# Performance work log

Measured on AMD Instinct MI355X. Metric: run time of the kernel, lower is better.

## Reference

```python
import jax, jax.numpy as jnp
import numpy as np

N_ITEMS = 100000
H = 256
L = 3
B = 512


def setup_inputs() -> dict:
    key = jax.random.key(0)
    ks = jax.random.split(key, 9)
    s = 1.0 / np.sqrt(H)  # PyTorch GRU/Linear default uniform bound
    return {
        "input": jax.random.randint(ks[0], (B,), 0, N_ITEMS),
        "hidden": jnp.zeros((L, B, H), jnp.float32),
        "W_ih0": jax.random.uniform(ks[1], (3 * H, N_ITEMS), jnp.float32, -s, s),
        "W_ih_hi": jax.random.uniform(ks[2], (L - 1, 3 * H, H), jnp.float32, -s, s),
        "W_hh": jax.random.uniform(ks[3], (L, 3 * H, H), jnp.float32, -s, s),
        "b_ih": jax.random.uniform(ks[4], (L, 3 * H), jnp.float32, -s, s),
        "b_hh": jax.random.uniform(ks[5], (L, 3 * H), jnp.float32, -s, s),
        "W_out": jax.random.uniform(ks[6], (N_ITEMS, H), jnp.float32, -s, s),
        "b_out": jax.random.uniform(ks[7], (N_ITEMS,), jnp.float32, -s, s),
    }


def _gru_cell(x_proj, h, W_hh_l, b_hh_l):
    # PyTorch GRU cell; x_proj already holds x @ W_ih.T + b_ih
    h_proj = h @ W_hh_l.T + b_hh_l
    xr, xz, xn = jnp.split(x_proj, 3, axis=-1)
    hr, hz, hn = jnp.split(h_proj, 3, axis=-1)
    r = jax.nn.sigmoid(xr + hr)
    z = jax.nn.sigmoid(xz + hz)
    n = jnp.tanh(xn + r * hn)
    return (1.0 - z) * n + z * h


def reference(input, hidden, W_ih0, W_ih_hi, W_hh, b_ih, b_hh, W_out, b_out):
    # one_hot(input) @ W_ih0.T == row-gather of W_ih0.T  (same math, no dense one-hot)
    x_proj = W_ih0.T[input] + b_ih[0]  # (B, 3H)
    x = _gru_cell(x_proj, hidden[0], W_hh[0], b_hh[0])
    new_h = [x]
    for l in range(1, L):  # fixed small layer loop
        x_proj = x @ W_ih_hi[l - 1].T + b_ih[l]
        x = _gru_cell(x_proj, hidden[l], W_hh[l], b_hh[l])
        new_h.append(x)
    h_new = jnp.stack(new_h)  # (L, B, H)
    activation = jnp.tanh(x @ W_out.T + b_out)  # (B, N_ITEMS)
    return activation, h_new
```

## Files before the change

### kernel.cpp

```cpp
#include <hip/hip_runtime.h>
#include <math.h>
#include <stdint.h>

#define NI 100000
#define NB 512
#define NH 256
#define H3 768

typedef _Float16 f16x8 __attribute__((ext_vector_type(8)));
typedef float    f32x4 __attribute__((ext_vector_type(4)));

__device__ __forceinline__ float tanh_fast(float x) {
    x = fminf(fmaxf(x, -9.0f), 9.0f);
    const float e = __expf(2.0f * x);
    return (e - 1.0f) * __builtin_amdgcn_rcpf(e + 1.0f);
}

__global__ void k_gates0(const int* __restrict__ idx,
                         const float* __restrict__ Wih0,
                         const float* __restrict__ bih0,
                         const float* __restrict__ hp,
                         const float* __restrict__ hprev,
                         float* __restrict__ hnew)
{
    const int b = blockIdx.x;
    const int j = threadIdx.x;
    const int ib = idx[b];
    const float xr = Wih0[(size_t)(j          ) * NI + ib] + bih0[j];
    const float xz = Wih0[(size_t)(j + NH     ) * NI + ib] + bih0[j + NH];
    const float xn = Wih0[(size_t)(j + 2 * NH ) * NI + ib] + bih0[j + 2 * NH];
    const float hr = hp[b * H3 + j];
    const float hz = hp[b * H3 + NH + j];
    const float hn = hp[b * H3 + 2 * NH + j];
    const float h  = hprev[b * NH + j];
    const float r = 1.0f / (1.0f + expf(-(xr + hr)));
    const float z = 1.0f / (1.0f + expf(-(xz + hz)));
    const float n = tanhf(xn + r * hn);
    hnew[b * NH + j] = (1.0f - z) * n + z * h;
}

__global__ void k_gates(const float* __restrict__ xp,
                        const float* __restrict__ hp,
                        const float* __restrict__ hprev,
                        float* __restrict__ hnew)
{
    const int b = blockIdx.x;
    const int j = threadIdx.x;
    const float xr = xp[b * H3 + j];
    const float xz = xp[b * H3 + NH + j];
    const float xn = xp[b * H3 + 2 * NH + j];
    const float hr = hp[b * H3 + j];
    const float hz = hp[b * H3 + NH + j];
    const float hn = hp[b * H3 + 2 * NH + j];
    const float h  = hprev[b * NH + j];
    const float r = 1.0f / (1.0f + expf(-(xr + hr)));
    const float z = 1.0f / (1.0f + expf(-(xz + hz)));
    const float n = tanhf(xn + r * hn);
    hnew[b * NH + j] = (1.0f - z) * n + z * h;
}

__global__ void k_gates_last(const float* __restrict__ xp,
                             const float* __restrict__ hp,
                             const float* __restrict__ hprev,
                             float* __restrict__ hnew,
                             _Float16* __restrict__ Xh)
{
    const int b = blockIdx.x;
    const int j = threadIdx.x;
    const float xr = xp[b * H3 + j];
    const float xz = xp[b * H3 + NH + j];
    const float xn = xp[b * H3 + 2 * NH + j];
    const float hr = hp[b * H3 + j];
    const float hz = hp[b * H3 + NH + j];
    const float hn = hp[b * H3 + 2 * NH + j];
    const float h  = hprev[b * NH + j];
    const float r = 1.0f / (1.0f + expf(-(xr + hr)));
    const float z = 1.0f / (1.0f + expf(-(xz + hz)));
    const float n = tanhf(xn + r * hn);
    const float v = (1.0f - z) * n + z * h;
    hnew[b * NH + j] = v;
    Xh[b * NH + j] = (_Float16)v;
}

__global__ __launch_bounds__(256)
void k_gemm_small(const float* __restrict__ A0,
                  const float* __restrict__ B0,
                  const float* __restrict__ bias0,
                  float* __restrict__ C0,
                  int M, int N, int K,
                  int sA, int sB, int sBias, int sC)
{
    constexpr int BM = 64, BN = 64, BK = 64;
    __shared__ float As[BK][BM];
    __shared__ float Bs[BK][BN];

    const float* A    = A0 + (size_t)blockIdx.z * sA;
    const float* Bm   = B0 + (size_t)blockIdx.z * sB;
    const float* bias = bias0 + (size_t)blockIdx.z * sBias;
    float*       C    = C0 + (size_t)blockIdx.z * sC;

    const int tid = threadIdx.x;
    const int tx  = tid & 15;
    const int ty  = tid >> 4;
    const int m0  = blockIdx.x * BM;
    const int n0  = blockIdx.y * BN;

    float acc[4][4];
#pragma unroll
    for (int i = 0; i < 4; i++)
#pragma unroll
        for (int j = 0; j < 4; j++) acc[i][j] = 0.0f;

    for (int k0 = 0; k0 < K; k0 += BK) {
#pragma unroll
        for (int f = 0; f < 4; f++) {
            const int fid = tid + f * 256;
            const int row = fid >> 4;
            const int t4  = fid & 15;
            const int mp  = row ^ ((t4 & 3) << 3);
            {
                const float4 v = *(const float4*)(A + (size_t)(m0 + row) * K + k0 + t4 * 4);
                As[t4 * 4 + 0][mp] = v.x; As[t4 * 4 + 1][mp] = v.y;
                As[t4 * 4 + 2][mp] = v.z; As[t4 * 4 + 3][mp] = v.w;
            }
            {
                const float4 v = *(const float4*)(Bm + (size_t)(n0 + row) * K + k0 + t4 * 4);
                Bs[t4 * 4 + 0][mp] = v.x; Bs[t4 * 4 + 1][mp] = v.y;
                Bs[t4 * 4 + 2][mp] = v.z; Bs[t4 * 4 + 3][mp] = v.w;
            }
        }
        __syncthreads();
#pragma unroll
        for (int kk = 0; kk < BK; kk++) {
            const int s = ((kk >> 2) & 3) << 3;
            const float4 a0 = *(const float4*)&As[kk][(ty * 4) ^ s];
            const float4 b0 = *(const float4*)&Bs[kk][(tx * 4) ^ s];
            const float av[4] = {a0.x, a0.y, a0.z, a0.w};
            const float bv[4] = {b0.x, b0.y, b0.z, b0.w};
#pragma unroll
            for (int i = 0; i < 4; i++)
#pragma unroll
                for (int j = 0; j < 4; j++)
                    acc[i][j] = fmaf(av[i], bv[j], acc[i][j]);
        }
        __syncthreads();
    }

#pragma unroll
    for (int i = 0; i < 4; i++) {
        const size_t rowoff = (size_t)(m0 + ty * 4 + i) * N;
        const int gn = n0 + tx * 4;
        const float4 bb = *(const float4*)(bias + gn);
        float4 v;
        v.x = acc[i][0] + bb.x; v.y = acc[i][1] + bb.y;
        v.z = acc[i][2] + bb.z; v.w = acc[i][3] + bb.w;
        *(float4*)(C + rowoff + gn) = v;
    }
}

__global__ __launch_bounds__(512, 4)
void k_out_mfma(const _Float16* __restrict__ Xh,
                const float* __restrict__ W,
                const float* __restrict__ bout,
                float* __restrict__ C)
{
    __shared__ __align__(16) float S[16384];

    const int n0   = blockIdx.x * 64;
    const int tid  = threadIdx.x;
    const int w    = tid >> 6;
    const int lane = tid & 63;
    const int lr   = lane & 15;
    const int lg   = lane >> 4;

#pragma unroll
    for (int it = 0; it < 8; ++it) {
        const int fid = it * 512 + tid;
        const int row = fid >> 6;
        const int p   = fid & 63;
        int gr = n0 + row; if (gr >= NI) gr = NI - 1;
        const float* src = W + (size_t)gr * NH + (size_t)(p ^ (row & 7)) * 4;
        __builtin_amdgcn_global_load_lds(
            (const __attribute__((address_space(1))) void*)src,
            (__attribute__((address_space(3))) void*)(S + fid * 4),
            16, 0, 0);
    }

    f32x4 acc[4][4];
#pragma unroll
    for (int nf = 0; nf < 4; ++nf)
#pragma unroll
        for (int mf = 0; mf < 4; ++mf) acc[nf][mf] = (f32x4){0.f, 0.f, 0.f, 0.f};

    __syncthreads();

    const _Float16* xbase = Xh + (size_t)(w * 64 + lr) * NH + lg * 8;

#pragma unroll
    for (int t = 0; t < 8; ++t) {
        f16x8 xf[4];
#pragma unroll
        for (int mf = 0; mf < 4; ++mf)
            xf[mf] = *(const f16x8*)(xbase + mf * 16 * NH + t * 32);
#pragma unroll
        for (int nf = 0; nf < 4; ++nf) {
            const int rl = nf * 16 + lr;
            const int c0 = t * 8 + ((lg * 2)     ^ (rl & 7));
            const int c1 = t * 8 + ((lg * 2 + 1) ^ (rl & 7));
            const f32x4 u0 = *(const f32x4*)(S + rl * 256 + c0 * 4);
            const f32x4 u1 = *(const f32x4*)(S + rl * 256 + c1 * 4);
            f16x8 h;
            h[0] = (_Float16)u0[0]; h[1] = (_Float16)u0[1];
            h[2] = (_Float16)u0[2]; h[3] = (_Float16)u0[3];
            h[4] = (_Float16)u1[0]; h[5] = (_Float16)u1[1];
            h[6] = (_Float16)u1[2]; h[7] = (_Float16)u1[3];
#pragma unroll
            for (int mf = 0; mf < 4; ++mf)
                acc[nf][mf] = __builtin_amdgcn_mfma_f32_16x16x32_f16(
                    h, xf[mf], acc[nf][mf], 0, 0, 0);
        }
    }

#pragma unroll
    for (int pass = 0; pass < 2; ++pass) {
        __syncthreads();
        if ((w >> 2) == pass) {
            const int mloc = (w & 3) * 64;
#pragma unroll
            for (int nf = 0; nf < 4; ++nf) {
                const int gn = n0 + nf * 16 + lg * 4;
                const float4 bb = (gn < NI) ? *(const float4*)(bout + gn)
                                            : make_float4(0.f, 0.f, 0.f, 0.f);
#pragma unroll
                for (int mf = 0; mf < 4; ++mf) {
                    const int mr = mloc + mf * 16 + lr;
                    const int p  = (nf * 4 + lg) ^ (lr & 7);
                    float4 v;
                    v.x = tanh_fast(acc[nf][mf][0] + bb.x);
                    v.y = tanh_fast(acc[nf][mf][1] + bb.y);
                    v.z = tanh_fast(acc[nf][mf][2] + bb.z);
                    v.w = tanh_fast(acc[nf][mf][3] + bb.w);
                    *(float4*)(S + mr * 64 + p * 4) = v;
                }
            }
        }
        __syncthreads();
#pragma unroll
        for (int it = 0; it < 8; ++it) {
            const int fid = it * 512 + tid;
            const int row = fid >> 4;
            const int c   = fid & 15;
            const int gn  = n0 + c * 4;
            if (gn < NI) {
                const f32x4 v = *(const f32x4*)(S + row * 64 + ((c ^ (row & 7)) * 4));
                __builtin_nontemporal_store(
                    v, (f32x4*)(C + (size_t)(pass * 256 + row) * NI + gn));
            }
        }
    }
}

extern "C" void kernel_launch(void* const* d_in, const int* in_sizes, int n_in,
                              void* d_out, int out_size, void* d_ws, size_t ws_size,
                              hipStream_t stream)
{
    const int*   idx    = (const int*)  d_in[0];
    const float* hidden = (const float*)d_in[1];
    const float* Wih0   = (const float*)d_in[2];
    const float* WihHi  = (const float*)d_in[3];
    const float* Whh    = (const float*)d_in[4];
    const float* bih    = (const float*)d_in[5];
    const float* bhh    = (const float*)d_in[6];
    const float* Wout   = (const float*)d_in[7];
    const float* bout   = (const float*)d_in[8];

    float* act  = (float*)d_out;
    float* hnew = act + (size_t)NB * NI;
    float* hp = act;
    float* xp = act + 3 * NB * H3;
    _Float16* Xh = (_Float16*)d_ws;

    const dim3 bs(256);
    const dim3 gs_hp(NB / 64, H3 / 64, 3);
    const dim3 gs_xp(NB / 64, H3 / 64, 1);

    k_gemm_small<<<gs_hp, bs, 0, stream>>>(hidden, Whh, bhh, hp,
                                           NB, H3, NH, NB * NH, H3 * NH, H3, NB * H3);
    k_gates0<<<NB, bs, 0, stream>>>(idx, Wih0, bih, hp, hidden, hnew);
    k_gemm_small<<<gs_xp, bs, 0, stream>>>(hnew, WihHi, bih + H3, xp,
                                           NB, H3, NH, 0, 0, 0, 0);
    k_gates<<<NB, bs, 0, stream>>>(xp, hp + NB * H3, hidden + NB * NH, hnew + NB * NH);
    k_gemm_small<<<gs_xp, bs, 0, stream>>>(hnew + NB * NH, WihHi + H3 * NH, bih + 2 * H3, xp,
                                           NB, H3, NH, 0, 0, 0, 0);
    k_gates_last<<<NB, bs, 0, stream>>>(xp, hp + 2 * NB * H3, hidden + 2 * NB * NH,
                                        hnew + 2 * NB * NH, Xh);

    k_out_mfma<<<dim3((NI + 63) / 64), dim3(512), 0, stream>>>(Xh, Wout, bout, act);
}
```

Before: 148.3 us.

## Fuse GRU gate math into layer GEMMs and retile output MFMA warps

Folds the layer-0 and layer-1 gate computations into the A-tile load of the following input-projection GEMM, removing two kernel launches and the round-trip of hnew through global memory. Each of the 12 column blocks recomputes the gates redundantly, and for layer 0 that includes strided gathers from the large embedding matrix. It also switches gate math to fast exp/tanh approximations. The output MFMA kernel is retiled so each warp covers 128 rows by 32 columns instead of 64 by 64, which cuts per-warp LDS weight reads and fp16 conversions but means more Xh loads from global.

```diff
diff --git a/kernel.cpp b/kernel.cpp
--- a/kernel.cpp
+++ b/kernel.cpp
@@ -15,34 +15,15 @@
     const float e = __expf(2.0f * x);
     return (e - 1.0f) * __builtin_amdgcn_rcpf(e + 1.0f);
 }
-
-__global__ void k_gates0(const int* __restrict__ idx,
-                         const float* __restrict__ Wih0,
-                         const float* __restrict__ bih0,
-                         const float* __restrict__ hp,
-                         const float* __restrict__ hprev,
-                         float* __restrict__ hnew)
-{
-    const int b = blockIdx.x;
-    const int j = threadIdx.x;
-    const int ib = idx[b];
-    const float xr = Wih0[(size_t)(j          ) * NI + ib] + bih0[j];
-    const float xz = Wih0[(size_t)(j + NH     ) * NI + ib] + bih0[j + NH];
-    const float xn = Wih0[(size_t)(j + 2 * NH ) * NI + ib] + bih0[j + 2 * NH];
-    const float hr = hp[b * H3 + j];
-    const float hz = hp[b * H3 + NH + j];
-    const float hn = hp[b * H3 + 2 * NH + j];
-    const float h  = hprev[b * NH + j];
-    const float r = 1.0f / (1.0f + expf(-(xr + hr)));
-    const float z = 1.0f / (1.0f + expf(-(xz + hz)));
-    const float n = tanhf(xn + r * hn);
-    hnew[b * NH + j] = (1.0f - z) * n + z * h;
-}
-
-__global__ void k_gates(const float* __restrict__ xp,
-                        const float* __restrict__ hp,
-                        const float* __restrict__ hprev,
-                        float* __restrict__ hnew)
+__device__ __forceinline__ float sigmoid_fast(float x) {
+    return 1.0f / (1.0f + __expf(-x));
+}
+
+__global__ void k_gates_last(const float* __restrict__ xp,
+                             const float* __restrict__ hp,
+                             const float* __restrict__ hprev,
+                             float* __restrict__ hnew,
+                             _Float16* __restrict__ Xh)
 {
     const int b = blockIdx.x;
     const int j = threadIdx.x;
@@ -53,30 +34,9 @@
     const float hz = hp[b * H3 + NH + j];
     const float hn = hp[b * H3 + 2 * NH + j];
     const float h  = hprev[b * NH + j];
-    const float r = 1.0f / (1.0f + expf(-(xr + hr)));
-    const float z = 1.0f / (1.0f + expf(-(xz + hz)));
-    const float n = tanhf(xn + r * hn);
-    hnew[b * NH + j] = (1.0f - z) * n + z * h;
-}
-
-__global__ void k_gates_last(const float* __restrict__ xp,
-                             const float* __restrict__ hp,
-                             const float* __restrict__ hprev,
-                             float* __restrict__ hnew,
-                             _Float16* __restrict__ Xh)
-{
-    const int b = blockIdx.x;
-    const int j = threadIdx.x;
-    const float xr = xp[b * H3 + j];
-    const float xz = xp[b * H3 + NH + j];
-    const float xn = xp[b * H3 + 2 * NH + j];
-    const float hr = hp[b * H3 + j];
-    const float hz = hp[b * H3 + NH + j];
-    const float hn = hp[b * H3 + 2 * NH + j];
-    const float h  = hprev[b * NH + j];
-    const float r = 1.0f / (1.0f + expf(-(xr + hr)));
-    const float z = 1.0f / (1.0f + expf(-(xz + hz)));
-    const float n = tanhf(xn + r * hn);
+    const float r = sigmoid_fast(xr + hr);
+    const float z = sigmoid_fast(xz + hz);
+    const float n = tanh_fast(xn + r * hn);
     const float v = (1.0f - z) * n + z * h;
     hnew[b * NH + j] = v;
     Xh[b * NH + j] = (_Float16)v;
@@ -158,6 +118,119 @@
     }
 }
 
+template<int MODE>
+__global__ __launch_bounds__(256)
+void k_gemm_fused(const int* __restrict__ idx,
+                  const float* __restrict__ Wih0,
+                  const float* __restrict__ bih0,
+                  const float* __restrict__ xprev,
+                  const float* __restrict__ hpl,
+                  const float* __restrict__ hprev,
+                  const float* __restrict__ Bm,
+                  const float* __restrict__ bias,
+                  float* __restrict__ hnew_out,
+                  float* __restrict__ xp_out)
+{
+    constexpr int BM = 64, BN = 64, BK = 64;
+    __shared__ float As[BK][BM];
+    __shared__ float Bs[BK][BN];
+
+    const int tid = threadIdx.x;
+    const int tx  = tid & 15;
+    const int ty  = tid >> 4;
+    const int m0  = blockIdx.x * BM;
+    const int n0  = blockIdx.y * BN;
+
+    float acc[4][4];
+#pragma unroll
+    for (int i = 0; i < 4; i++)
+#pragma unroll
+        for (int j = 0; j < 4; j++) acc[i][j] = 0.0f;
+
+    for (int k0 = 0; k0 < NH; k0 += BK) {
+#pragma unroll
+        for (int f = 0; f < 4; f++) {
+            const int fid = tid + f * 256;
+            const int row = fid >> 4;
+            const int t4  = fid & 15;
+            const int mp  = row ^ ((t4 & 3) << 3);
+            const int b   = m0 + row;
+            const int j0  = k0 + t4 * 4;
+
+            float xr[4], xz[4], xn[4];
+            if (MODE == 0) {
+                const int ib = idx[b];
+#pragma unroll
+                for (int e = 0; e < 4; e++) {
+                    xr[e] = Wih0[(size_t)(j0 + e) * NI + ib]          + bih0[j0 + e];
+                    xz[e] = Wih0[(size_t)(j0 + e + NH) * NI + ib]     + bih0[j0 + e + NH];
+                    xn[e] = Wih0[(size_t)(j0 + e + 2 * NH) * NI + ib] + bih0[j0 + e + 2 * NH];
+                }
+            } else {
+                const float4 a = *(const float4*)(xprev + (size_t)b * H3 + j0);
+                const float4 c = *(const float4*)(xprev + (size_t)b * H3 + NH + j0);
+                const float4 d = *(const float4*)(xprev + (size_t)b * H3 + 2 * NH + j0);
+                xr[0]=a.x; xr[1]=a.y; xr[2]=a.z; xr[3]=a.w;
+                xz[0]=c.x; xz[1]=c.y; xz[2]=c.z; xz[3]=c.w;
+                xn[0]=d.x; xn[1]=d.y; xn[2]=d.z; xn[3]=d.w;
+            }
+            const float4 hr4 = *(const float4*)(hpl + (size_t)b * H3 + j0);
+            const float4 hz4 = *(const float4*)(hpl + (size_t)b * H3 + NH + j0);
+            const float4 hn4 = *(const float4*)(hpl + (size_t)b * H3 + 2 * NH + j0);
+            const float4 h4  = *(const float4*)(hprev + (size_t)b * NH + j0);
+            const float hr[4] = {hr4.x, hr4.y, hr4.z, hr4.w};
+            const float hz[4] = {hz4.x, hz4.y, hz4.z, hz4.w};
+            const float hn[4] = {hn4.x, hn4.y, hn4.z, hn4.w};
+            const float hh[4] = {h4.x, h4.y, h4.z, h4.w};
+            float av[4];
+#pragma unroll
+            for (int e = 0; e < 4; e++) {
+                const float r = sigmoid_fast(xr[e] + hr[e]);
+                const float z = sigmoid_fast(xz[e] + hz[e]);
+                const float n = tanh_fast(xn[e] + r * hn[e]);
+                av[e] = (1.0f - z) * n + z * hh[e];
+            }
+            As[t4 * 4 + 0][mp] = av[0]; As[t4 * 4 + 1][mp] = av[1];
+            As[t4 * 4 + 2][mp] = av[2]; As[t4 * 4 + 3][mp] = av[3];
+            if (n0 == 0) {
+                float4 o; o.x = av[0]; o.y = av[1]; o.z = av[2]; o.w = av[3];
+                *(float4*)(hnew_out + (size_t)b * NH + j0) = o;
+            }
+            {
+                const float4 v = *(const float4*)(Bm + (size_t)(n0 + row) * NH + k0 + t4 * 4);
+                Bs[t4 * 4 + 0][mp] = v.x; Bs[t4 * 4 + 1][mp] = v.y;
+                Bs[t4 * 4 + 2][mp] = v.z; Bs[t4 * 4 + 3][mp] = v.w;
+            }
+        }
+        __syncthreads();
+#pragma unroll
+        for (int kk = 0; kk < BK; kk++) {
+            const int s = ((kk >> 2) & 3) << 3;
+            const float4 a0 = *(const float4*)&As[kk][(ty * 4) ^ s];
+            const float4 b0 = *(const float4*)&Bs[kk][(tx * 4) ^ s];
+            const float av[4] = {a0.x, a0.y, a0.z, a0.w};
+            const float bv[4] = {b0.x, b0.y, b0.z, b0.w};
+#pragma unroll
+            for (int i = 0; i < 4; i++)
+#pragma unroll
+                for (int j = 0; j < 4; j++)
+                    acc[i][j] = fmaf(av[i], bv[j], acc[i][j]);
+        }
+        __syncthreads();
+    }
+
+#pragma unroll
+    for (int i = 0; i < 4; i++) {
+        const size_t rowoff = (size_t)(m0 + ty * 4 + i) * H3;
+        const int gn = n0 + tx * 4;
+        const float4 bb = *(const float4*)(bias + gn);
+        float4 v;
+        v.x = acc[i][0] + bb.x; v.y = acc[i][1] + bb.y;
+        v.z = acc[i][2] + bb.z; v.w = acc[i][3] + bb.w;
+        *(float4*)(xp_out + rowoff + gn) = v;
+    }
+}
+
 __global__ __launch_bounds__(512, 4)
 void k_out_mfma(const _Float16* __restrict__ Xh,
                 const float* __restrict__ W,
@@ -172,39 +245,39 @@
     const int lane = tid & 63;
     const int lr   = lane & 15;
     const int lg   = lane >> 4;
+    const int p    = w >> 2;
+    const int wmh  = (w >> 1) & 1;
+    const int wn2  = w & 1;
 
 #pragma unroll
     for (int it = 0; it < 8; ++it) {
         const int fid = it * 512 + tid;
         const int row = fid >> 6;
-        const int p   = fid & 63;
+        const int pc  = fid & 63;
         int gr = n0 + row; if (gr >= NI) gr = NI - 1;
-        const float* src = W + (size_t)gr * NH + (size_t)(p ^ (row & 7)) * 4;
+        const float* src = W + (size_t)gr * NH + (size_t)(pc ^ (row & 7)) * 4;
         __builtin_amdgcn_global_load_lds(
             (const __attribute__((address_space(1))) void*)src,
             (__attribute__((address_space(3))) void*)(S + fid * 4),
             16, 0, 0);
     }
 
-    f32x4 acc[4][4];
-#pragma unroll
-    for (int nf = 0; nf < 4; ++nf)
-#pragma unroll
-        for (int mf = 0; mf < 4; ++mf) acc[nf][mf] = (f32x4){0.f, 0.f, 0.f, 0.f};
+    f32x4 acc[2][8];
+#pragma unroll
+    for (int nf = 0; nf < 2; ++nf)
+#pragma unroll
+        for (int mf = 0; mf < 8; ++mf) acc[nf][mf] = (f32x4){0.f, 0.f, 0.f, 0.f};
 
     __syncthreads();
 
-    const _Float16* xbase = Xh + (size_t)(w * 64 + lr) * NH + lg * 8;
+    const _Float16* xbase = Xh + (size_t)(p * 256 + wmh * 128 + lr) * NH + lg * 8;
 
 #pragma unroll
     for (int t = 0; t < 8; ++t) {
-        f16x8 xf[4];
-#pragma unroll
-        for (int mf = 0; mf < 4; ++mf)
-            xf[mf] = *(const f16x8*)(xbase + mf * 16 * NH + t * 32);
-#pragma unroll
-        for (int nf = 0; nf < 4; ++nf) {
-            const int rl = nf * 16 + lr;
+        f16x8 wf[2];
+#pragma unroll
+        for (int nf = 0; nf < 2; ++nf) {
+            const int rl = wn2 * 32 + nf * 16 + lr;
             const int c0 = t * 8 + ((lg * 2)     ^ (rl & 7));
             const int c1 = t * 8 + ((lg * 2 + 1) ^ (rl & 7));
             const f32x4 u0 = *(const f32x4*)(S + rl * 256 + c0 * 4);
@@ -214,33 +287,36 @@
             h[2] = (_Float16)u0[2]; h[3] = (_Float16)u0[3];
             h[4] = (_Float16)u1[0]; h[5] = (_Float16)u1[1];
             h[6] = (_Float16)u1[2]; h[7] = (_Float16)u1[3];
-#pragma unroll
-            for (int mf = 0; mf < 4; ++mf)
-                acc[nf][mf] = __builtin_amdgcn_mfma_f32_16x16x32_f16(
-                    h, xf[mf], acc[nf][mf], 0, 0, 0);
+            wf[nf] = h;
+        }
+#pragma unroll
+        for (int mf = 0; mf < 8; ++mf) {
+            const f16x8 xf = *(const f16x8*)(xbase + mf * 16 * NH + t * 32);
+            acc[0][mf] = __builtin_amdgcn_mfma_f32_16x16x32_f16(wf[0], xf, acc[0][mf], 0, 0, 0);
+            acc[1][mf] = __builtin_amdgcn_mfma_f32_16x16x32_f16(wf[1], xf, acc[1][mf], 0, 0, 0);
         }
     }
 
 #pragma unroll
     for (int pass = 0; pass < 2; ++pass) {
         __syncthreads();
-        if ((w >> 2) == pass) {
-            const int mloc = (w & 3) * 64;
-#pragma unroll
-            for (int nf = 0; nf < 4; ++nf) {
-                const int gn = n0 + nf * 16 + lg * 4;
+        if (p == pass) {
+#pragma unroll
+            for (int nf = 0; nf < 2; ++nf) {
+                const int gn = n0 + wn2 * 32 + nf * 16 + lg * 4;
                 const float4 bb = (gn < NI) ? *(const float4*)(bout + gn)
                                             : make_float4(0.f, 0.f, 0.f, 0.f);
-#pragma unroll
-                for (int mf = 0; mf < 4; ++mf) {
-                    const int mr = mloc + mf * 16 + lr;
-                    const int p  = (nf * 4 + lg) ^ (lr & 7);
+                const int q = wn2 * 8 + nf * 4 + lg;
+#pragma unroll
+                for (int mf = 0; mf < 8; ++mf) {
+                    const int mr   = wmh * 128 + mf * 16 + lr;
+                    const int slot = q ^ (lr & 7);
                     float4 v;
                     v.x = tanh_fast(acc[nf][mf][0] + bb.x);
                     v.y = tanh_fast(acc[nf][mf][1] + bb.y);
                     v.z = tanh_fast(acc[nf][mf][2] + bb.z);
                     v.w = tanh_fast(acc[nf][mf][3] + bb.w);
-                    *(float4*)(S + mr * 64 + p * 4) = v;
+                    *(float4*)(S + mr * 64 + slot * 4) = v;
                 }
             }
         }
@@ -276,8 +352,9 @@
 
     float* act  = (float*)d_out;
     float* hnew = act + (size_t)NB * NI;
-    float* hp = act;
-    float* xp = act + 3 * NB * H3;
+    float* hp  = act;
+    float* xp1 = act + 3 * NB * H3;
+    float* xp2 = xp1 + NB * H3;
     _Float16* Xh = (_Float16*)d_ws;
 
     const dim3 bs(256);
@@ -286,14 +363,14 @@
 
     k_gemm_small<<<gs_hp, bs, 0, stream>>>(hidden, Whh, bhh, hp,
                                            NB, H3, NH, NB * NH, H3 * NH, H3, NB * H3);
-    k_gates0<<<NB, bs, 0, stream>>>(idx, Wih0, bih, hp, hidden, hnew);
-    k_gemm_small<<<gs_xp, bs, 0, stream>>>(hnew, WihHi, bih + H3, xp,
-                                           NB, H3, NH, 0, 0, 0, 0);
-    k_gates<<<NB, bs, 0, stream>>>(xp, hp + NB * H3, hidden + NB * NH, hnew + NB * NH);
-    k_gemm_small<<<gs_xp, bs, 0, stream>>>(hnew + NB * NH, WihHi + H3 * NH, bih + 2 * H3, xp,
-                                           NB, H3, NH, 0, 0, 0, 0);
-    k_gates_last<<<NB, bs, 0, stream>>>(xp, hp + 2 * NB * H3, hidden + 2 * NB * NH,
+    k_gemm_fused<0><<<gs_xp, bs, 0, stream>>>(idx, Wih0, bih, nullptr,
+                                              hp, hidden, WihHi, bih + H3,
+                                              hnew, xp1);
+    k_gemm_fused<1><<<gs_xp, bs, 0, stream>>>(nullptr, nullptr, nullptr, xp1,
+                                              hp + NB * H3, hidden + NB * NH,
+                                              WihHi + H3 * NH, bih + 2 * H3,
+                                              hnew + NB * NH, xp2);
+    k_gates_last<<<NB, bs, 0, stream>>>(xp2, hp + 2 * NB * H3, hidden + 2 * NB * NH,
                                         hnew + 2 * NB * NH, Xh);
-
     k_out_mfma<<<dim3((NI + 63) / 64), dim3(512), 0, stream>>>(Xh, Wout, bout, act);
 }
```

After: 251.5 us. 69.6% more time.
